# Optimization experiments

Hardware: AMD Instinct MI355X
Metric: run time of the kernel (lower is better)

## Reference

```python
import jax, jax.numpy as jnp
import numpy as np

NEG_SLOPE = 0.2
EPS = 1e-16


def gat_layer(x, edge_index, edge_attr, W, We, a_src, a_dst, a_edge, bias,
              add_self_loops):
    """PyG GATConv with concat=True.
    x: [N, F_in], edge_index: [2, E] (row 0 = src j, row 1 = dst i),
    edge_attr: [E, De], W: [F_in, H*C], We: [De, H*C],
    a_src/a_dst/a_edge: [H, C], bias: [H*C].
    """
    N = x.shape[0]
    H, C = a_src.shape
    if add_self_loops:
        # fill_value='mean': self-loop edge_attr = mean of incoming edge_attr per node
        dst0 = edge_index[1]
        s = jax.ops.segment_sum(edge_attr, dst0, num_segments=N)
        cnt = jax.ops.segment_sum(jnp.ones((edge_attr.shape[0], 1), edge_attr.dtype),
                                  dst0, num_segments=N)
        loop_attr = s / jnp.maximum(cnt, 1.0)
        loop_idx = jnp.arange(N, dtype=edge_index.dtype)
        edge_index = jnp.concatenate(
            [edge_index, jnp.stack([loop_idx, loop_idx])], axis=1)
        edge_attr = jnp.concatenate([edge_attr, loop_attr], axis=0)

    src, dst = edge_index[0], edge_index[1]
    h = (x @ W).reshape(N, H, C)                       # [N, H, C]
    e = (edge_attr @ We).reshape(-1, H, C)             # [E, H, C]

    alpha_src = jnp.einsum('nhc,hc->nh', h, a_src)     # [N, H]
    alpha_dst = jnp.einsum('nhc,hc->nh', h, a_dst)     # [N, H]
    alpha_edge = jnp.einsum('ehc,hc->eh', e, a_edge)   # [E, H]

    alpha = alpha_src[src] + alpha_dst[dst] + alpha_edge
    alpha = jax.nn.leaky_relu(alpha, NEG_SLOPE)

    # segment softmax over destination node
    amax = jax.ops.segment_max(alpha, dst, num_segments=N)      # [N, H]
    ex = jnp.exp(alpha - amax[dst])
    denom = jax.ops.segment_sum(ex, dst, num_segments=N)        # [N, H]
    attn = ex / (denom[dst] + EPS)                               # [E, H]

    msg = h[src] * attn[:, :, None]                              # [E, H, C]
    out = jax.ops.segment_sum(msg, dst, num_segments=N)          # [N, H, C]
    return out.reshape(N, H * C) + bias


def setup_inputs() -> dict:
    key = jax.random.key(0)
    ks = jax.random.split(key, 16)
    N, E, F_in, C, H, De = 10000, 160000, 128, 64, 8, 1
    d1 = H * C  # 512

    def glorot(k, shape):
        fan = shape[0] + shape[-1]
        s = jnp.sqrt(6.0 / fan)
        return jax.random.uniform(k, shape, jnp.float32, -s, s)

    return {
        'x': jax.random.normal(ks[0], (N, F_in), jnp.float32),
        'edge_index': jax.random.randint(ks[1], (2, E), 0, N, jnp.int32),
        'edge_attr': jax.random.normal(ks[2], (E, De), jnp.float32),
        # layer 1 params
        'W1': glorot(ks[3], (F_in, d1)),
        'We1': glorot(ks[4], (De, d1)),
        'as1': glorot(ks[5], (H, C)),
        'ad1': glorot(ks[6], (H, C)),
        'ae1': glorot(ks[7], (H, C)),
        'b1': jnp.zeros((d1,), jnp.float32),
        # layer 2 params
        'W2': glorot(ks[8], (d1, d1)),
        'We2': glorot(ks[9], (De, d1)),
        'as2': glorot(ks[10], (H, C)),
        'ad2': glorot(ks[11], (H, C)),
        'ae2': glorot(ks[12], (H, C)),
        'b2': jnp.zeros((d1,), jnp.float32),
    }


def reference(x, edge_index, edge_attr,
              W1, We1, as1, ad1, ae1, b1,
              W2, We2, as2, ad2, ae2, b2):
    h = gat_layer(x, edge_index, edge_attr, W1, We1, as1, ad1, ae1, b1,
                  add_self_loops=False)
    h = jax.nn.relu(h)
    h = gat_layer(h, edge_index, edge_attr, W2, We2, as2, ad2, ae2, b2,
                  add_self_loops=True)
    return jnp.mean(h, axis=0)  # [512]
```

## Files before the change

### kernel.cpp

```cpp
#include <hip/hip_runtime.h>
#include <hip/hip_bf16.h>

#define HD __device__ __forceinline__
typedef unsigned short u16;
typedef __attribute__((ext_vector_type(8))) short bf16x8;
typedef __attribute__((ext_vector_type(4))) float f32x4;

HD u16 f2b(float f){
  unsigned u = __float_as_uint(f);
  unsigned r = (u + 0x7fffu + ((u>>16)&1u)) >> 16;
  return (u16)r;
}
HD float b2f(short s){ return __uint_as_float(((unsigned)(u16)s)<<16); }

template<int AF32>
HD void gemm_body(const void* Ap, const u16* __restrict__ Bt,
                  u16* __restrict__ Cb,
                  const float* __restrict__ a_s, const float* __restrict__ a_d,
                  float* __restrict__ asrc, float* __restrict__ adst,
                  int M, int N, int K, int bidx, int bidy, char* lds){
  char* As = lds;
  char* Bs = lds + 128*80;
  const int tid = threadIdx.x;
  const int lane = tid & 63, w = tid >> 6;
  const int wr = w >> 1, wc = w & 1;
  const int l15 = lane & 15, l4 = lane >> 4;
  const int m0 = bidy*128, n0 = bidx*128;

  f32x4 acc[4][4] = {};
  int aoff[4], boff[4];
  #pragma unroll
  for (int i=0;i<4;++i) aoff[i] = (wr*64 + i*16 + l15)*80 + l4*16;
  #pragma unroll
  for (int j=0;j<4;++j) boff[j] = (wc*64 + j*16 + l15)*80 + l4*16;

  for (int k0=0; k0<K; k0+=32){
    #pragma unroll
    for (int i=0;i<2;++i){
      int cid = tid*2+i;
      int r = cid>>2, c = cid&3;
      int row = m0 + r;
      if (AF32){
        const float* A = (const float*)Ap;
        float4 v0 = make_float4(0.f,0.f,0.f,0.f), v1 = v0;
        if (row < M){
          v0 = *(const float4*)(A + (size_t)row*K + k0 + c*8);
          v1 = *(const float4*)(A + (size_t)row*K + k0 + c*8 + 4);
        }
        ushort4 o0, o1;
        o0.x=f2b(v0.x); o0.y=f2b(v0.y); o0.z=f2b(v0.z); o0.w=f2b(v0.w);
        o1.x=f2b(v1.x); o1.y=f2b(v1.y); o1.z=f2b(v1.z); o1.w=f2b(v1.w);
        *(ushort4*)(As + r*80 + c*16)     = o0;
        *(ushort4*)(As + r*80 + c*16 + 8) = o1;
      } else {
        const u16* A = (const u16*)Ap;
        float4 v = make_float4(0.f,0.f,0.f,0.f);
        if (row < M) v = *(const float4*)(A + (size_t)row*K + k0 + c*8);
        *(float4*)(As + r*80 + c*16) = v;
      }
    }
    #pragma unroll
    for (int i=0;i<2;++i){
      int cid = tid*2+i;
      int r = cid>>2, c = cid&3;
      float4 v = *(const float4*)(Bt + (size_t)(n0+r)*K + k0 + c*8);
      *(float4*)(Bs + r*80 + c*16) = v;
    }
    __syncthreads();
    bf16x8 a[4], b[4];
    #pragma unroll
    for (int i=0;i<4;++i) a[i] = *reinterpret_cast<const bf16x8*>(As + aoff[i]);
    #pragma unroll
    for (int j=0;j<4;++j) b[j] = *reinterpret_cast<const bf16x8*>(Bs + boff[j]);
    #pragma unroll
    for (int i=0;i<4;++i)
      #pragma unroll
      for (int j=0;j<4;++j)
        acc[i][j] = __builtin_amdgcn_mfma_f32_16x16x32_bf16(a[i], b[j], acc[i][j], 0,0,0);
    __syncthreads();
  }

  const int head = (n0>>6) + wc;
  float sv[4][4] = {}, dv[4][4] = {};
  #pragma unroll
  for (int i=0;i<4;++i){
    #pragma unroll
    for (int j=0;j<4;++j){
      int col = n0 + wc*64 + j*16 + l15;
      float asv = a_s[col], adv = a_d[col];
      #pragma unroll
      for (int r=0;r<4;++r){
        int row = m0 + wr*64 + i*16 + l4*4 + r;
        u16 bits = f2b(acc[i][j][r]);
        float valf = b2f((short)bits);
        if (row < M) Cb[(size_t)row*N + col] = bits;
        sv[i][r] = fmaf(valf, asv, sv[i][r]);
        dv[i][r] = fmaf(valf, adv, dv[i][r]);
      }
    }
  }
  #pragma unroll
  for (int i=0;i<4;++i){
    #pragma unroll
    for (int r=0;r<4;++r){
      float s_ = sv[i][r], d_ = dv[i][r];
      #pragma unroll
      for (int mask=1; mask<16; mask<<=1){
        s_ += __shfl_xor(s_, mask);
        d_ += __shfl_xor(d_, mask);
      }
      if (l15==0){
        int row = m0 + wr*64 + i*16 + l4*4 + r;
        if (row < M){ asrc[row*8+head] = s_; adst[row*8+head] = d_; }
      }
    }
  }
}

__global__ __launch_bounds__(256) void k_prepA(
    const int* __restrict__ dst, const float* __restrict__ ea,
    int* cnt, float* easum, int E, int nbCount,
    const float* __restrict__ W1, u16* __restrict__ W1t,
    const float* __restrict__ W2, u16* __restrict__ W2t,
    const float* __restrict__ We1, const float* __restrict__ ae1,
    const float* __restrict__ We2, const float* __restrict__ ae2,
    float* wedot){
  __shared__ float T[64][65];
  int bx = blockIdx.x;
  int tid = threadIdx.x;
  if (bx < nbCount){
    int e = bx*256 + tid;
    if (e<E){
      int d = dst[e];
      atomicAdd(&cnt[d],1);
      atomicAdd(&easum[d], ea[e]);
    }
    return;
  }
  bx -= nbCount;
  if (bx < 16 + 64){
    const float* W; u16* Wt; int K, t;
    if (bx < 16){ t = bx;      W = W1; Wt = W1t; K = 128; }
    else        { t = bx - 16; W = W2; Wt = W2t; K = 512; }
    const int Nn = 512, nt = 8;
    int k0 = (t/nt)*64, n0 = (t%nt)*64;
    #pragma unroll
    for (int i=0;i<16;++i){
      int id = i*256 + tid;
      int r = id>>6, c = id&63;
      T[r][c] = W[(size_t)(k0+r)*Nn + n0 + c];
    }
    __syncthreads();
    #pragma unroll
    for (int i=0;i<16;++i){
      int id = i*256 + tid;
      int rr = id>>6, cc = id&63;
      Wt[(size_t)(n0+rr)*K + k0 + cc] = f2b(T[cc][rr]);
    }
    return;
  }
  int idx = bx - 80;
  int which = idx>>1, hg = idx&1;
  const float* We = which? We2 : We1;
  const float* ae = which? ae2 : ae1;
  int wv = tid>>6, lane = tid&63;
  int head = hg*4 + wv;
  float p = We[head*64+lane]*ae[head*64+lane];
  #pragma unroll
  for (int o=32;o;o>>=1) p += __shfl_down(p,o);
  if (lane==0) wedot[which*8+head] = p;
}

__global__ __launch_bounds__(256) void k_prepB(
    const int* __restrict__ cnt, int* offs, int N, int nbLa,
    const float* __restrict__ easum, float* la,
    const float* __restrict__ x, const u16* __restrict__ W1t,
    u16* __restrict__ hb1,
    const float* __restrict__ a_s, const float* __restrict__ a_d,
    float* __restrict__ asrc, float* __restrict__ adst,
    int M, int Nd, int K){
  __shared__ char glds[256*80];
  __shared__ int slds[256];
  int bx = blockIdx.x;
  int tid = threadIdx.x;
  if (bx == 0){
    const int chunk = (N + 255)/256;
    const int b = tid*chunk;
    int s = 0;
    for (int i=0;i<chunk;++i){ int idx=b+i; if (idx<N) s += cnt[idx]; }
    slds[tid] = s;
    __syncthreads();
    #pragma unroll
    for (int off=1; off<256; off<<=1){
      int t = (tid>=off)? slds[tid-off] : 0;
      __syncthreads();
      slds[tid] += t;
      __syncthreads();
    }
    int excl = slds[tid] - s;
    for (int i=0;i<chunk;++i){
      int idx=b+i;
      if (idx<N){ offs[idx] = excl; excl += cnt[idx]; }
    }
    if (tid==255) offs[N] = slds[255];
    return;
  }
  if (bx < 1 + nbLa){
    int n = (bx-1)*256 + tid;
    if (n<N) la[n] = easum[n] / fmaxf((float)cnt[n], 1.f);
    return;
  }
  int t = bx - 1 - nbLa;
  gemm_body<1>(x, W1t, hb1, a_s, a_d, asrc, adst, M, Nd, K, t%4, t/4, glds);
}

__global__ void k_scatter(const int* __restrict__ src, const int* __restrict__ dst,
                          const float* __restrict__ ea, const int* __restrict__ offs,
                          int* fill, int* srcs, float* eas, int E){
  int e = blockIdx.x*blockDim.x + threadIdx.x;
  if (e>=E) return;
  int d = dst[e];
  int p = offs[d] + atomicAdd(&fill[d],1);
  srcs[p] = src[e];
  eas[p]  = ea[e];
}

__global__ __launch_bounds__(256) void k_gemm_mfma(
    const u16* __restrict__ A, const u16* __restrict__ Bt,
    u16* __restrict__ Cb,
    const float* __restrict__ a_s, const float* __restrict__ a_d,
    float* __restrict__ asrc, float* __restrict__ adst,
    int M, int N, int K){
  __shared__ char lds[256*80];
  gemm_body<0>(A, Bt, Cb, a_s, a_d, asrc, adst, M, N, K,
               blockIdx.x, blockIdx.y, lds);
}

__global__ __launch_bounds__(256) void k_flashagg(const u16* __restrict__ hb,
    const int* __restrict__ srcs, const float* __restrict__ eas,
    const int* __restrict__ offs,
    const float* __restrict__ asrc, const float* __restrict__ adst,
    const float* __restrict__ wedot, const float* __restrict__ la,
    const float* __restrict__ bias,
    u16* __restrict__ outb,
    int N, int relu_flag, int self_flag){
  int n = blockIdx.x*4 + (threadIdx.x>>6);
  if (n>=N) return;
  int lane = threadIdx.x&63;
  int hh = lane&7, esub = lane>>3;
  int ahh = lane>>3;
  int c0 = lane*8;
  int beg = offs[n], end = offs[n+1];
  float wd = wedot[hh];
  float adn = adst[n*8+hh];

  float aselfa = -1e30f;
  if (self_flag){
    float a = asrc[n*8+hh] + adn + la[n]*wd;
    aselfa = a>0.f ? a : 0.2f*a;
  }
  float aself_c = __shfl(aselfa, ahh);

  float m = self_flag ? aself_c : -1e30f;
  float s = 0.f;
  float acc[8] = {};

  for (int p0=beg; p0<end; p0+=16){
    int pA = p0 + esub, pB = p0 + 8 + esub;
    float aA = -1e30f, aB = -1e30f;
    int sA = 0, sB = 0;
    if (pA < end){
      sA = srcs[pA];
      float eaA = eas[pA];
      float a = asrc[sA*8+hh] + adn + eaA*wd;
      aA = a>0.f ? a : 0.2f*a;
    }
    if (pB < end){
      sB = srcs[pB];
      float eaB = eas[pB];
      float a = asrc[sB*8+hh] + adn + eaB*wd;
      aB = a>0.f ? a : 0.2f*a;
    }
    float av[16]; int se[16];
    #pragma unroll
    for (int e=0;e<8;++e){ av[e]   = __shfl(aA, e*8 + ahh); se[e]   = __shfl(sA, e*8); }
    #pragma unroll
    for (int e=0;e<8;++e){ av[8+e] = __shfl(aB, e*8 + ahh); se[8+e] = __shfl(sB, e*8); }
    float mo = m;
    #pragma unroll
    for (int e=0;e<16;++e) mo = fmaxf(mo, av[e]);
    float f = __expf(m - mo);
    m = mo;
    s *= f;
    #pragma unroll
    for (int j=0;j<8;++j) acc[j] *= f;
    #pragma unroll
    for (int e=0;e<16;++e){
      if (p0 + e < end){
        float ee = __expf(av[e] - m);
        s += ee;
        bf16x8 v = *(const bf16x8*)(hb + (size_t)se[e]*512 + c0);
        #pragma unroll
        for (int j=0;j<8;++j) acc[j] = fmaf(ee, b2f(v[j]), acc[j]);
      }
    }
  }
  if (self_flag){
    float xs = __expf(aself_c - m);
    s += xs;
    bf16x8 v = *(const bf16x8*)(hb + (size_t)n*512 + c0);
    #pragma unroll
    for (int j=0;j<8;++j) acc[j] = fmaf(xs, b2f(v[j]), acc[j]);
  }
  float iv = 1.f/(s + 1e-16f);
  bf16x8 ov;
  #pragma unroll
  for (int j=0;j<8;++j){
    float val = acc[j]*iv + bias[c0+j];
    if (relu_flag) val = fmaxf(val, 0.f);
    ov[j] = (short)f2b(val);
  }
  *(bf16x8*)(outb + (size_t)n*512 + c0) = ov;
}

__global__ __launch_bounds__(512) void k_colmean(const u16* __restrict__ out2b,
                          float* __restrict__ o, int N, float invN){
  int c = threadIdx.x;
  int n0 = blockIdx.x*16;
  int nend = min(n0+16, N);
  float s = 0.f;
  for (int n=n0;n<nend;++n) s += b2f(out2b[(size_t)n*512 + c]);
  atomicAdd(&o[c], s*invN);
}

extern "C" void kernel_launch(void* const* d_in, const int* in_sizes, int n_in,
                              void* d_out, int out_size, void* d_ws, size_t ws_size,
                              hipStream_t stream){
  const float* x   = (const float*)d_in[0];
  const int* eidx  = (const int*)d_in[1];
  const float* ea  = (const float*)d_in[2];
  const float* W1  = (const float*)d_in[3];
  const float* We1 = (const float*)d_in[4];
  const float* as1 = (const float*)d_in[5];
  const float* ad1 = (const float*)d_in[6];
  const float* ae1 = (const float*)d_in[7];
  const float* b1  = (const float*)d_in[8];
  const float* W2  = (const float*)d_in[9];
  const float* We2 = (const float*)d_in[10];
  const float* as2 = (const float*)d_in[11];
  const float* ad2 = (const float*)d_in[12];
  const float* ae2 = (const float*)d_in[13];
  const float* b2  = (const float*)d_in[14];
  float* outp = (float*)d_out;

  const int FIN = 128, D1 = 512;
  const int N = in_sizes[0]/FIN;
  const int E = in_sizes[1]/2;
  const int* srcA = eidx;
  const int* dstA = eidx + E;

  char* ws = (char*)d_ws;
  size_t o = 0;
  auto alloc = [&](size_t bytes)->void*{
    void* p = ws + o; o = (o + bytes + 255) & ~(size_t)255; return p;
  };
  u16*   hb1   = (u16*)  alloc((size_t)N*D1*2);
  u16*   hb2   = (u16*)  alloc((size_t)N*D1*2);
  u16*   out1rb= (u16*)  alloc((size_t)N*D1*2);
  u16*   out2b = (u16*)  alloc((size_t)N*D1*2);
  u16*   W1t   = (u16*)  alloc((size_t)D1*FIN*2);
  u16*   W2t   = (u16*)  alloc((size_t)D1*D1*2);
  int*   srcs  = (int*)  alloc((size_t)E*4);
  float* eas   = (float*)alloc((size_t)E*4);
  int*   offs  = (int*)  alloc((size_t)(N+1)*4);
  size_t zbeg = o;
  int*   cnt   = (int*)  alloc((size_t)N*4);
  int*   fill  = (int*)  alloc((size_t)N*4);
  float* easum = (float*)alloc((size_t)N*4);
  size_t zend = o;
  float* asrc  = (float*)alloc((size_t)N*8*4);
  float* adst  = (float*)alloc((size_t)N*8*4);
  float* la    = (float*)alloc((size_t)N*4);
  float* wedot = (float*)alloc(64);
  (void)ws_size; (void)n_in;

  hipMemsetAsync(ws + zbeg, 0, zend - zbeg, stream);
  hipMemsetAsync(d_out, 0, (size_t)out_size*sizeof(float), stream);

  dim3 b256(256);
  int ge = (E+255)/256;
  int gn4 = (N+3)/4;

  int nbCount = ge;
  k_prepA<<<nbCount + 16 + 64 + 4, b256, 0, stream>>>(
      dstA, ea, cnt, easum, E, nbCount,
      W1, W1t, W2, W2t, We1, ae1, We2, ae2, wedot);

  int nbLa = (N+255)/256;
  int nbG1 = (D1/128)*((N+127)/128);
  k_prepB<<<1 + nbLa + nbG1, b256, 0, stream>>>(
      cnt, offs, N, nbLa, easum, la,
      x, W1t, hb1, as1, ad1, asrc, adst, N, D1, FIN);

  k_scatter<<<ge, b256, 0, stream>>>(srcA, dstA, ea, offs, fill, srcs, eas, E);

  k_flashagg<<<gn4, b256, 0, stream>>>(hb1, srcs, eas, offs, asrc, adst, wedot, la,
                                       b1, out1rb, N, 1, 0);

  k_gemm_mfma<<<dim3(D1/128, (N+127)/128), b256, 0, stream>>>(
      out1rb, W2t, hb2, as2, ad2, asrc, adst, N, D1, D1);

  k_flashagg<<<gn4, b256, 0, stream>>>(hb2, srcs, eas, offs, asrc, adst, wedot+8, la,
                                       b2, out2b, N, 0, 1);

  k_colmean<<<(N+15)/16, 512, 0, stream>>>(out2b, outp, N, 1.0f/(float)N);
}
```

Baseline: 175.2 us.

## Split aggregation into per-head-pair channel slices and fuse scatter with layer-1 GEMM

The edge-aggregation kernel now gives each wave a 128-channel slice (two heads) of one node instead of all 512 channels. That is four times as many waves, each processing 32 edges per step and loading 4 bytes per lane rather than 16. Block indices are interleaved so the four slices of the same node group run close together, which should help L2 reuse of the gathered rows. The CSR scatter now runs in the same kernel as the layer-1 GEMM, and the prefix scan and loop-attribute computation get their own small kernel. The trade-off is that softmax logits are recomputed once per slice and each gather is narrower, which could cost more than the added parallelism gains.

```diff
diff --git a/kernel.cpp b/kernel.cpp
--- a/kernel.cpp
+++ b/kernel.cpp
@@ -171,15 +171,9 @@
   if (lane==0) wedot[which*8+head] = p;
 }
 
-__global__ __launch_bounds__(256) void k_prepB(
-    const int* __restrict__ cnt, int* offs, int N, int nbLa,
-    const float* __restrict__ easum, float* la,
-    const float* __restrict__ x, const u16* __restrict__ W1t,
-    u16* __restrict__ hb1,
-    const float* __restrict__ a_s, const float* __restrict__ a_d,
-    float* __restrict__ asrc, float* __restrict__ adst,
-    int M, int Nd, int K){
-  __shared__ char glds[256*80];
+__global__ __launch_bounds__(256) void k_scanla(
+    const int* __restrict__ cnt, int* offs, int N,
+    const float* __restrict__ easum, float* la){
   __shared__ int slds[256];
   int bx = blockIdx.x;
   int tid = threadIdx.x;
@@ -205,24 +199,33 @@
     if (tid==255) offs[N] = slds[255];
     return;
   }
-  if (bx < 1 + nbLa){
-    int n = (bx-1)*256 + tid;
-    if (n<N) la[n] = easum[n] / fmaxf((float)cnt[n], 1.f);
+  int n = (bx-1)*256 + tid;
+  if (n<N) la[n] = easum[n] / fmaxf((float)cnt[n], 1.f);
+}
+
+__global__ __launch_bounds__(256) void k_scatgemm(
+    const int* __restrict__ src, const int* __restrict__ dst,
+    const float* __restrict__ ea, const int* __restrict__ offs,
+    int* fill, int* srcs, float* eas, int E, int nbScat,
+    const float* __restrict__ x, const u16* __restrict__ W1t,
+    u16* __restrict__ hb1,
+    const float* __restrict__ a_s, const float* __restrict__ a_d,
+    float* __restrict__ asrc, float* __restrict__ adst,
+    int M, int Nd, int K){
+  __shared__ char glds[256*80];
+  int bx = blockIdx.x;
+  if (bx < nbScat){
+    int e = bx*256 + threadIdx.x;
+    if (e<E){
+      int d = dst[e];
+      int p = offs[d] + atomicAdd(&fill[d],1);
+      srcs[p] = src[e];
+      eas[p]  = ea[e];
+    }
     return;
   }
-  int t = bx - 1 - nbLa;
+  int t = bx - nbScat;
   gemm_body<1>(x, W1t, hb1, a_s, a_d, asrc, adst, M, Nd, K, t%4, t/4, glds);
-}
-
-__global__ void k_scatter(const int* __restrict__ src, const int* __restrict__ dst,
-                          const float* __restrict__ ea, const int* __restrict__ offs,
-                          int* fill, int* srcs, float* eas, int E){
-  int e = blockIdx.x*blockDim.x + threadIdx.x;
-  if (e>=E) return;
-  int d = dst[e];
-  int p = offs[d] + atomicAdd(&fill[d],1);
-  srcs[p] = src[e];
-  eas[p]  = ea[e];
 }
 
 __global__ __launch_bounds__(256) void k_gemm_mfma(
@@ -243,84 +246,73 @@
     const float* __restrict__ wedot, const float* __restrict__ la,
     const float* __restrict__ bias,
     u16* __restrict__ outb,
-    int N, int relu_flag, int self_flag){
-  int n = blockIdx.x*4 + (threadIdx.x>>6);
-  if (n>=N) return;
-  int lane = threadIdx.x&63;
-  int hh = lane&7, esub = lane>>3;
-  int ahh = lane>>3;
-  int c0 = lane*8;
+    int N, int G, int relu_flag, int self_flag){
+  int b = blockIdx.x;
+  int slice = (b & 7) >> 1, sub = b & 1;
+  int g = (b >> 3)*2 + sub;
+  if (g >= G) return;
+  int n = g*4 + (int)(threadIdx.x >> 6);
+  if (n >= N) return;
+  int lane = threadIdx.x & 63;
+  int hp = slice*2 + (lane & 1);
+  int myh = slice*2 + (lane >> 5);
+  int hb_ = lane >> 5;
+  int c0 = slice*128 + lane*2;
   int beg = offs[n], end = offs[n+1];
-  float wd = wedot[hh];
-  float adn = adst[n*8+hh];
+  float wd_p = wedot[hp];
+  float adn_p = adst[n*8+hp];
 
   float aselfa = -1e30f;
   if (self_flag){
-    float a = asrc[n*8+hh] + adn + la[n]*wd;
+    float a = asrc[n*8+myh] + adst[n*8+myh] + la[n]*wedot[myh];
     aselfa = a>0.f ? a : 0.2f*a;
   }
-  float aself_c = __shfl(aselfa, ahh);
-
-  float m = self_flag ? aself_c : -1e30f;
+  float m = self_flag ? aselfa : -1e30f;
   float s = 0.f;
-  float acc[8] = {};
-
-  for (int p0=beg; p0<end; p0+=16){
-    int pA = p0 + esub, pB = p0 + 8 + esub;
-    float aA = -1e30f, aB = -1e30f;
-    int sA = 0, sB = 0;
-    if (pA < end){
-      sA = srcs[pA];
-      float eaA = eas[pA];
-      float a = asrc[sA*8+hh] + adn + eaA*wd;
-      aA = a>0.f ? a : 0.2f*a;
-    }
-    if (pB < end){
-      sB = srcs[pB];
-      float eaB = eas[pB];
-      float a = asrc[sB*8+hh] + adn + eaB*wd;
-      aB = a>0.f ? a : 0.2f*a;
-    }
-    float av[16]; int se[16];
-    #pragma unroll
-    for (int e=0;e<8;++e){ av[e]   = __shfl(aA, e*8 + ahh); se[e]   = __shfl(sA, e*8); }
-    #pragma unroll
-    for (int e=0;e<8;++e){ av[8+e] = __shfl(aB, e*8 + ahh); se[8+e] = __shfl(sB, e*8); }
+  float acc0 = 0.f, acc1 = 0.f;
+
+  for (int p0=beg; p0<end; p0+=32){
+    int p = p0 + (lane>>1);
+    float a = -1e30f; int sp = 0;
+    if (p < end){
+      sp = srcs[p];
+      float a0 = asrc[sp*8+hp] + adn_p + eas[p]*wd_p;
+      a = a0>0.f ? a0 : 0.2f*a0;
+    }
+    float av[32]; int se[32];
+    #pragma unroll
+    for (int e=0;e<32;++e){ av[e] = __shfl(a, e*2 + hb_); se[e] = __shfl(sp, e*2); }
     float mo = m;
     #pragma unroll
-    for (int e=0;e<16;++e) mo = fmaxf(mo, av[e]);
+    for (int e=0;e<32;++e) mo = fmaxf(mo, av[e]);
     float f = __expf(m - mo);
     m = mo;
-    s *= f;
-    #pragma unroll
-    for (int j=0;j<8;++j) acc[j] *= f;
-    #pragma unroll
-    for (int e=0;e<16;++e){
+    s *= f; acc0 *= f; acc1 *= f;
+    #pragma unroll
+    for (int e=0;e<32;++e){
       if (p0 + e < end){
         float ee = __expf(av[e] - m);
         s += ee;
-        bf16x8 v = *(const bf16x8*)(hb + (size_t)se[e]*512 + c0);
-        #pragma unroll
-        for (int j=0;j<8;++j) acc[j] = fmaf(ee, b2f(v[j]), acc[j]);
+        unsigned two = *(const unsigned*)(hb + (size_t)se[e]*512 + c0);
+        acc0 = fmaf(ee, b2f((short)(two & 0xffff)), acc0);
+        acc1 = fmaf(ee, b2f((short)(two >> 16)), acc1);
       }
     }
   }
   if (self_flag){
-    float xs = __expf(aself_c - m);
+    float xs = __expf(aselfa - m);
     s += xs;
-    bf16x8 v = *(const bf16x8*)(hb + (size_t)n*512 + c0);
-    #pragma unroll
-    for (int j=0;j<8;++j) acc[j] = fmaf(xs, b2f(v[j]), acc[j]);
+    unsigned two = *(const unsigned*)(hb + (size_t)n*512 + c0);
+    acc0 = fmaf(xs, b2f((short)(two & 0xffff)), acc0);
+    acc1 = fmaf(xs, b2f((short)(two >> 16)), acc1);
   }
   float iv = 1.f/(s + 1e-16f);
-  bf16x8 ov;
-  #pragma unroll
-  for (int j=0;j<8;++j){
-    float val = acc[j]*iv + bias[c0+j];
-    if (relu_flag) val = fmaxf(val, 0.f);
-    ov[j] = (short)f2b(val);
-  }
-  *(bf16x8*)(outb + (size_t)n*512 + c0) = ov;
+  float2 bv = *(const float2*)(bias + c0);
+  float v0 = acc0*iv + bv.x;
+  float v1 = acc1*iv + bv.y;
+  if (relu_flag){ v0 = fmaxf(v0,0.f); v1 = fmaxf(v1,0.f); }
+  unsigned ou = ((unsigned)f2b(v1)<<16) | f2b(v0);
+  *(unsigned*)(outb + (size_t)n*512 + c0) = ou;
 }
 
 __global__ __launch_bounds__(512) void k_colmean(const u16* __restrict__ out2b,
@@ -389,29 +381,28 @@
 
   dim3 b256(256);
   int ge = (E+255)/256;
-  int gn4 = (N+3)/4;
-
-  int nbCount = ge;
-  k_prepA<<<nbCount + 16 + 64 + 4, b256, 0, stream>>>(
-      dstA, ea, cnt, easum, E, nbCount,
+  int G  = (N+3)/4;
+  int nbFA = 8*((G+1)/2);
+
+  k_prepA<<<ge + 16 + 64 + 4, b256, 0, stream>>>(
+      dstA, ea, cnt, easum, E, ge,
       W1, W1t, W2, W2t, We1, ae1, We2, ae2, wedot);
 
-  int nbLa = (N+255)/256;
+  k_scanla<<<1 + (N+255)/256, b256, 0, stream>>>(cnt, offs, N, easum, la);
+
   int nbG1 = (D1/128)*((N+127)/128);
-  k_prepB<<<1 + nbLa + nbG1, b256, 0, stream>>>(
-      cnt, offs, N, nbLa, easum, la,
+  k_scatgemm<<<ge + nbG1, b256, 0, stream>>>(
+      srcA, dstA, ea, offs, fill, srcs, eas, E, ge,
       x, W1t, hb1, as1, ad1, asrc, adst, N, D1, FIN);
 
-  k_scatter<<<ge, b256, 0, stream>>>(srcA, dstA, ea, offs, fill, srcs, eas, E);
-
-  k_flashagg<<<gn4, b256, 0, stream>>>(hb1, srcs, eas, offs, asrc, adst, wedot, la,
-                                       b1, out1rb, N, 1, 0);
+  k_flashagg<<<nbFA, b256, 0, stream>>>(hb1, srcs, eas, offs, asrc, adst,
+                                        wedot, la, b1, out1rb, N, G, 1, 0);
 
   k_gemm_mfma<<<dim3(D1/128, (N+127)/128), b256, 0, stream>>>(
       out1rb, W2t, hb2, as2, ad2, asrc, adst, N, D1, D1);
 
-  k_flashagg<<<gn4, b256, 0, stream>>>(hb2, srcs, eas, offs, asrc, adst, wedot+8, la,
-                                       b2, out2b, N, 0, 1);
+  k_flashagg<<<nbFA, b256, 0, stream>>>(hb2, srcs, eas, offs, asrc, adst,
+                                        wedot+8, la, b2, out2b, N, G, 0, 1);
 
   k_colmean<<<(N+15)/16, 512, 0, stream>>>(out2b, outp, N, 1.0f/(float)N);
 }
```

Result: slower. 260.5 us (+48.7%).

## Fuse edge scatter with layer-1 GEMM and batch gathers in aggregation

Applied to the files above, without the earlier changes.

The small prefix-scan and loop-attr work moves into its own kernel. The edge scatter now shares one launch with the layer-1 MFMA GEMM, so the scatter's atomic and irregular-store work can run alongside the GEMM blocks. The aggregation kernel gets a separate unguarded path for full 16-edge chunks that issues all 16 feature-row gathers before consuming them, raising memory-level parallelism. Partial chunks fall back to the guarded loop. The cost is higher register pressure from holding 16 bf16x8 vectors, which may lower occupancy.

```diff
diff --git a/kernel.cpp b/kernel.cpp
--- a/kernel.cpp
+++ b/kernel.cpp
@@ -171,15 +171,9 @@
   if (lane==0) wedot[which*8+head] = p;
 }
 
-__global__ __launch_bounds__(256) void k_prepB(
-    const int* __restrict__ cnt, int* offs, int N, int nbLa,
-    const float* __restrict__ easum, float* la,
-    const float* __restrict__ x, const u16* __restrict__ W1t,
-    u16* __restrict__ hb1,
-    const float* __restrict__ a_s, const float* __restrict__ a_d,
-    float* __restrict__ asrc, float* __restrict__ adst,
-    int M, int Nd, int K){
-  __shared__ char glds[256*80];
+__global__ __launch_bounds__(256) void k_scanla(
+    const int* __restrict__ cnt, int* offs, int N,
+    const float* __restrict__ easum, float* la){
   __shared__ int slds[256];
   int bx = blockIdx.x;
   int tid = threadIdx.x;
@@ -205,24 +199,33 @@
     if (tid==255) offs[N] = slds[255];
     return;
   }
-  if (bx < 1 + nbLa){
-    int n = (bx-1)*256 + tid;
-    if (n<N) la[n] = easum[n] / fmaxf((float)cnt[n], 1.f);
+  int n = (bx-1)*256 + tid;
+  if (n<N) la[n] = easum[n] / fmaxf((float)cnt[n], 1.f);
+}
+
+__global__ __launch_bounds__(256) void k_scatgemm(
+    const int* __restrict__ src, const int* __restrict__ dst,
+    const float* __restrict__ ea, const int* __restrict__ offs,
+    int* fill, int* srcs, float* eas, int E, int nbScat,
+    const float* __restrict__ x, const u16* __restrict__ W1t,
+    u16* __restrict__ hb1,
+    const float* __restrict__ a_s, const float* __restrict__ a_d,
+    float* __restrict__ asrc, float* __restrict__ adst,
+    int M, int Nd, int K){
+  __shared__ char glds[256*80];
+  int bx = blockIdx.x;
+  if (bx < nbScat){
+    int e = bx*256 + threadIdx.x;
+    if (e<E){
+      int d = dst[e];
+      int p = offs[d] + atomicAdd(&fill[d],1);
+      srcs[p] = src[e];
+      eas[p]  = ea[e];
+    }
     return;
   }
-  int t = bx - 1 - nbLa;
+  int t = bx - nbScat;
   gemm_body<1>(x, W1t, hb1, a_s, a_d, asrc, adst, M, Nd, K, t%4, t/4, glds);
-}
-
-__global__ void k_scatter(const int* __restrict__ src, const int* __restrict__ dst,
-                          const float* __restrict__ ea, const int* __restrict__ offs,
-                          int* fill, int* srcs, float* eas, int E){
-  int e = blockIdx.x*blockDim.x + threadIdx.x;
-  if (e>=E) return;
-  int d = dst[e];
-  int p = offs[d] + atomicAdd(&fill[d],1);
-  srcs[p] = src[e];
-  eas[p]  = ea[e];
 }
 
 __global__ __launch_bounds__(256) void k_gemm_mfma(
@@ -265,21 +268,54 @@
   float s = 0.f;
   float acc[8] = {};
 
-  for (int p0=beg; p0<end; p0+=16){
+  int nfull = (end - beg) & ~15;
+  int pend_full = beg + nfull;
+  int p0 = beg;
+
+  for (; p0 < pend_full; p0 += 16){
+    int pA = p0 + esub, pB = pA + 8;
+    int sA = srcs[pA], sB = srcs[pB];
+    float eaA = eas[pA], eaB = eas[pB];
+    float aA = asrc[sA*8+hh] + adn + eaA*wd;  aA = aA>0.f ? aA : 0.2f*aA;
+    float aB = asrc[sB*8+hh] + adn + eaB*wd;  aB = aB>0.f ? aB : 0.2f*aB;
+    float av[16]; int se[16];
+    #pragma unroll
+    for (int e=0;e<8;++e){ av[e]   = __shfl(aA, e*8 + ahh); se[e]   = __shfl(sA, e*8); }
+    #pragma unroll
+    for (int e=0;e<8;++e){ av[8+e] = __shfl(aB, e*8 + ahh); se[8+e] = __shfl(sB, e*8); }
+    float mo = m;
+    #pragma unroll
+    for (int e=0;e<16;++e) mo = fmaxf(mo, av[e]);
+    float f = __expf(m - mo);
+    m = mo;
+    s *= f;
+    #pragma unroll
+    for (int j=0;j<8;++j) acc[j] *= f;
+    bf16x8 v[16];
+    #pragma unroll
+    for (int e=0;e<16;++e) v[e] = *(const bf16x8*)(hb + (size_t)se[e]*512 + c0);
+    #pragma unroll
+    for (int e=0;e<16;++e){
+      float ee = __expf(av[e] - m);
+      s += ee;
+      #pragma unroll
+      for (int j=0;j<8;++j) acc[j] = fmaf(ee, b2f(v[e][j]), acc[j]);
+    }
+  }
+
+  if (p0 < end){
     int pA = p0 + esub, pB = p0 + 8 + esub;
     float aA = -1e30f, aB = -1e30f;
     int sA = 0, sB = 0;
     if (pA < end){
       sA = srcs[pA];
-      float eaA = eas[pA];
-      float a = asrc[sA*8+hh] + adn + eaA*wd;
-      aA = a>0.f ? a : 0.2f*a;
+      float a0 = asrc[sA*8+hh] + adn + eas[pA]*wd;
+      aA = a0>0.f ? a0 : 0.2f*a0;
     }
     if (pB < end){
       sB = srcs[pB];
-      float eaB = eas[pB];
-      float a = asrc[sB*8+hh] + adn + eaB*wd;
-      aB = a>0.f ? a : 0.2f*a;
+      float a0 = asrc[sB*8+hh] + adn + eas[pB]*wd;
+      aB = a0>0.f ? a0 : 0.2f*a0;
     }
     float av[16]; int se[16];
     #pragma unroll
@@ -299,18 +335,19 @@
       if (p0 + e < end){
         float ee = __expf(av[e] - m);
         s += ee;
-        bf16x8 v = *(const bf16x8*)(hb + (size_t)se[e]*512 + c0);
+        bf16x8 v0 = *(const bf16x8*)(hb + (size_t)se[e]*512 + c0);
         #pragma unroll
-        for (int j=0;j<8;++j) acc[j] = fmaf(ee, b2f(v[j]), acc[j]);
+        for (int j=0;j<8;++j) acc[j] = fmaf(ee, b2f(v0[j]), acc[j]);
       }
     }
   }
+
   if (self_flag){
     float xs = __expf(aself_c - m);
     s += xs;
-    bf16x8 v = *(const bf16x8*)(hb + (size_t)n*512 + c0);
-    #pragma unroll
-    for (int j=0;j<8;++j) acc[j] = fmaf(xs, b2f(v[j]), acc[j]);
+    bf16x8 v0 = *(const bf16x8*)(hb + (size_t)n*512 + c0);
+    #pragma unroll
+    for (int j=0;j<8;++j) acc[j] = fmaf(xs, b2f(v0[j]), acc[j]);
   }
   float iv = 1.f/(s + 1e-16f);
   bf16x8 ov;
@@ -391,27 +428,25 @@
   int ge = (E+255)/256;
   int gn4 = (N+3)/4;
 
-  int nbCount = ge;
-  k_prepA<<<nbCount + 16 + 64 + 4, b256, 0, stream>>>(
-      dstA, ea, cnt, easum, E, nbCount,
+  k_prepA<<<ge + 16 + 64 + 4, b256, 0, stream>>>(
+      dstA, ea, cnt, easum, E, ge,
       W1, W1t, W2, W2t, We1, ae1, We2, ae2, wedot);
 
-  int nbLa = (N+255)/256;
+  k_scanla<<<1 + (N+255)/256, b256, 0, stream>>>(cnt, offs, N, easum, la);
+
   int nbG1 = (D1/128)*((N+127)/128);
-  k_prepB<<<1 + nbLa + nbG1, b256, 0, stream>>>(
-      cnt, offs, N, nbLa, easum, la,
+  k_scatgemm<<<ge + nbG1, b256, 0, stream>>>(
+      srcA, dstA, ea, offs, fill, srcs, eas, E, ge,
       x, W1t, hb1, as1, ad1, asrc, adst, N, D1, FIN);
 
-  k_scatter<<<ge, b256, 0, stream>>>(srcA, dstA, ea, offs, fill, srcs, eas, E);
-
-  k_flashagg<<<gn4, b256, 0, stream>>>(hb1, srcs, eas, offs, asrc, adst, wedot, la,
-                                       b1, out1rb, N, 1, 0);
+  k_flashagg<<<gn4, b256, 0, stream>>>(hb1, srcs, eas, offs, asrc, adst,
+                                       wedot, la, b1, out1rb, N, 1, 0);
 
   k_gemm_mfma<<<dim3(D1/128, (N+127)/128), b256, 0, stream>>>(
       out1rb, W2t, hb2, as2, ad2, asrc, adst, N, D1, D1);
 
-  k_flashagg<<<gn4, b256, 0, stream>>>(hb2, srcs, eas, offs, asrc, adst, wedot+8, la,
-                                       b2, out2b, N, 0, 1);
+  k_flashagg<<<gn4, b256, 0, stream>>>(hb2, srcs, eas, offs, asrc, adst,
+                                       wedot+8, la, b2, out2b, N, 0, 1);
 
   k_colmean<<<(N+15)/16, 512, 0, stream>>>(out2b, outp, N, 1.0f/(float)N);
 }
```

After: 183.8 us. 1.05x slower.
